# Optimization experiments

Hardware: AMD Instinct MI355X
Metric: run time of the kernel (lower is better)

Reference implementation:

```python
import jax, jax.numpy as jnp
import numpy as np

D_MODEL = 2048
N_HEADS = 16
D_HEAD = D_MODEL // N_HEADS
FF = 4 * D_MODEL
B, L = 2, 2048


def setup_inputs() -> dict:
    key = jax.random.key(0)
    ks = jax.random.split(key, 12)
    s = 0.02
    inp = {
        "x": jax.random.normal(ks[0], (B, L, D_MODEL), jnp.float32),
        "rope_cos": jnp.cos(jnp.arange(L)[:, None] / (10000.0 ** (jnp.arange(D_HEAD) / D_HEAD))).astype(jnp.float32),
        "rope_sin": jnp.sin(jnp.arange(L)[:, None] / (10000.0 ** (jnp.arange(D_HEAD) / D_HEAD))).astype(jnp.float32),
        "mask": jnp.ones((B, L), jnp.int32),
        "w_norm1": jnp.ones((D_MODEL,), jnp.float32),
        "w_norm2": jnp.ones((D_MODEL,), jnp.float32),
        # linear weights stored as [in, out] (transposed torch layout)
        "wq": jax.random.normal(ks[1], (D_MODEL, D_MODEL), jnp.float32) * s,
        "wk": jax.random.normal(ks[2], (D_MODEL, D_MODEL), jnp.float32) * s,
        "wv": jax.random.normal(ks[3], (D_MODEL, D_MODEL), jnp.float32) * s,
        "wo": jax.random.normal(ks[4], (D_MODEL, D_MODEL), jnp.float32) * s,
        "w_ff1": jax.random.normal(ks[5], (D_MODEL, FF), jnp.float32) * s,
        "w_ff2": jax.random.normal(ks[6], (FF, D_MODEL), jnp.float32) * s,
    }
    return inp


def _rmsnorm(x, w):
    eps = jnp.finfo(x.dtype).eps
    return x * jax.lax.rsqrt(jnp.mean(x * x, axis=-1, keepdims=True) + eps) * w


def _rotate_half(x):
    x1, x2 = jnp.split(x, 2, axis=-1)
    return jnp.concatenate([-x2, x1], axis=-1)


def reference(x, rope_cos, rope_sin, mask, w_norm1, w_norm2, wq, wk, wv, wo, w_ff1, w_ff2):
    b, l, d = x.shape
    h, dh = N_HEADS, D_HEAD

    residual = x
    xn = _rmsnorm(x, w_norm1)
    # project and split heads: [B, H, L, DH]
    q = (xn @ wq).reshape(b, l, h, dh).transpose(0, 2, 1, 3)
    k = (xn @ wk).reshape(b, l, h, dh).transpose(0, 2, 1, 3)
    v = (xn @ wv).reshape(b, l, h, dh).transpose(0, 2, 1, 3)

    cos = rope_cos[None, None]  # [1,1,L,DH]
    sin = rope_sin[None, None]
    q = q * cos + _rotate_half(q) * sin
    k = k * cos + _rotate_half(k) * sin

    scores = jnp.einsum("bhqd,bhkd->bhqk", q, k) * (dh ** -0.5)
    causal = jnp.tril(jnp.ones((l, l), bool))  # allowed positions
    allowed = causal[None, None] & (mask[:, None, None, :] != 0)
    scores = jnp.where(allowed, scores, -jnp.inf)
    attn = jax.nn.softmax(scores, axis=-1)  # dropout is identity in eval

    out = jnp.einsum("bhqk,bhkd->bhqd", attn, v)
    out = out.transpose(0, 2, 1, 3).reshape(b, l, d)
    x = residual + out @ wo

    xn2 = _rmsnorm(x, w_norm2)
    ff = jax.nn.silu(xn2 @ w_ff1) @ w_ff2
    return x + ff
```

## Files before the change

kernel.cpp:

```cpp
#include <hip/hip_runtime.h>


typedef __bf16 bf16;
typedef __bf16 bf16x8 __attribute__((ext_vector_type(8)));
typedef float  f32x4  __attribute__((ext_vector_type(4)));

__device__ __forceinline__ void gload16(const void* g, void* l) {
  __builtin_amdgcn_global_load_lds((const __attribute__((address_space(1))) void*)g,
                                   (__attribute__((address_space(3))) void*)l,
                                   16, 0, 0);
}

#define CBAR asm volatile("" ::: "memory")
#define WAITV(N) asm volatile("s_waitcnt vmcnt(" #N ")" ::: "memory")
#define LGKM0 asm volatile("s_waitcnt lgkmcnt(0)" ::: "memory")
#define BARR { CBAR; __builtin_amdgcn_s_barrier(); CBAR; }

__global__ __launch_bounds__(256) void rmsnorm_to_bf16(
    const float* __restrict__ x, const float* __restrict__ w, bf16* __restrict__ out)
{
  const int D = 2048;
  const int row = blockIdx.x;
  const int tid = threadIdx.x;
  const float* xr = x + (size_t)row * D;
  float4 a = ((const float4*)xr)[tid * 2];
  float4 c = ((const float4*)xr)[tid * 2 + 1];
  float ss = a.x*a.x + a.y*a.y + a.z*a.z + a.w*a.w
           + c.x*c.x + c.y*c.y + c.z*c.z + c.w*c.w;
  #pragma unroll
  for (int m = 1; m < 64; m <<= 1) ss += __shfl_xor(ss, m, 64);
  __shared__ float red[4];
  if ((tid & 63) == 0) red[tid >> 6] = ss;
  __syncthreads();
  float tot = red[0] + red[1] + red[2] + red[3];
  float rms = rsqrtf(tot * (1.0f / D) + 1.1920929e-7f);
  const float* wr = w + tid * 8;
  float vals[8] = {a.x, a.y, a.z, a.w, c.x, c.y, c.z, c.w};
  bf16x8 o;
  #pragma unroll
  for (int j = 0; j < 8; ++j) o[j] = (bf16)(vals[j] * rms * wr[j]);
  *(bf16x8*)(out + (size_t)row * D + tid * 8) = o;
}

__global__ __launch_bounds__(256) void transpose_to_bf16(
    const float* __restrict__ in, bf16* __restrict__ out, int R, int C)
{
  __shared__ float tile[32][33];
  const int tx = threadIdx.x, ty = threadIdx.y;
  const int c0 = blockIdx.x * 32, r0 = blockIdx.y * 32;
  #pragma unroll
  for (int i = 0; i < 4; ++i)
    tile[ty + i * 8][tx] = in[(size_t)(r0 + ty + i * 8) * C + c0 + tx];
  __syncthreads();
  #pragma unroll
  for (int i = 0; i < 4; ++i)
    out[(size_t)(c0 + ty + i * 8) * R + r0 + tx] = (bf16)tile[tx][ty + i * 8];
}

__global__ __launch_bounds__(256) void v_transpose(
    const bf16* __restrict__ v, bf16* __restrict__ vt)
{
  const int L = 2048, DM = 2048;
  __shared__ bf16 tile[32][33];
  const int tx = threadIdx.x, ty = threadIdx.y;
  const int k0 = blockIdx.x * 32;
  const int d0 = blockIdx.y * 32;
  const int bh = blockIdx.z;
  const int b = bh >> 4, h = bh & 15;
  #pragma unroll
  for (int i = 0; i < 4; ++i)
    tile[ty + i * 8][tx] = v[(size_t)(b * L + k0 + ty + i * 8) * DM + h * 128 + d0 + tx];
  __syncthreads();
  #pragma unroll
  for (int i = 0; i < 4; ++i) {
    const int d = d0 + ty + i * 8;
    const int key = k0 + tx;
    const int keysw = (key & ~63) | (((((key >> 3) & 7) ^ (d & 7)) << 3)) | (key & 7);
    vt[(size_t)(bh * 128 + d) * L + keysw] = tile[tx][ty + i * 8];
  }
}

template<int EPI>
__global__ __launch_bounds__(512, 2) void gemm256(
    const bf16* __restrict__ A, const bf16* __restrict__ Bt,
    void* Cout, const float* __restrict__ resid, int M, int N, int K)
{
  __shared__ bf16 sA[2][2][128 * 64];
  __shared__ bf16 sB[2][2][128 * 64];

  const int tid = threadIdx.x, lane = tid & 63, w = tid >> 6;
  const int wm = w >> 2, wn = w & 3;
  const int lo = lane & 15, hi = lane >> 4;
  const int lo7 = lo & 7;

  const int nbn = N >> 8;
  const int nwg = gridDim.x;
  int swz = blockIdx.x;
  if ((nwg & 7) == 0) { const int cpx = nwg >> 3; swz = (swz & 7) * cpx + (swz >> 3); }
  const int bm = swz / nbn, bn = swz % nbn;

  const int r0 = tid >> 3,         s0 = (tid & 7) ^ (r0 & 7);
  const int r1 = (512 + tid) >> 3, s1 = ((512 + tid) & 7) ^ (r1 & 7);
  const bf16* Ab = A  + (size_t)(bm * 256) * K;
  const bf16* Bb = Bt + (size_t)(bn * 256) * K;
  const size_t o0 = (size_t)r0 * K + s0 * 8;
  const size_t o1 = (size_t)r1 * K + s1 * 8;
  const int dst0 = (w * 64) * 8, dst1 = (512 + w * 64) * 8;
  const size_t rhK = (size_t)128 * K;

  bf16x8 afA[2][4], b0[2][2], b1[2][2];
  f32x4 acc[8][4] = {};
  const int NT = K >> 6;

  auto stageA = [&](int b, int rh, int kt) {
    const bf16* s = Ab + rh * rhK + (size_t)kt * 64;
    gload16(s + o0, &sA[b][rh][dst0]);
    gload16(s + o1, &sA[b][rh][dst1]);
  };
  auto stageB = [&](int b, int rh, int kt) {
    const bf16* s = Bb + rh * rhK + (size_t)kt * 64;
    gload16(s + o0, &sB[b][rh][dst0]);
    gload16(s + o1, &sB[b][rh][dst1]);
  };
  auto loadA = [&](int b, int rh) {
    #pragma unroll
    for (int ks = 0; ks < 2; ++ks)
      #pragma unroll
      for (int m = 0; m < 4; ++m) {
        const int row = wm * 64 + m * 16 + lo;
        afA[ks][m] = *(const bf16x8*)&sA[b][rh][row * 64 + (((ks * 4 + hi) ^ lo7) << 3)];
      }
  };
  auto loadB = [&](bf16x8 (&d)[2][2], int b, int rh) {
    #pragma unroll
    for (int ks = 0; ks < 2; ++ks)
      #pragma unroll
      for (int nj = 0; nj < 2; ++nj) {
        const int row = wn * 32 + nj * 16 + lo;
        d[ks][nj] = *(const bf16x8*)&sB[b][rh][row * 64 + (((ks * 4 + hi) ^ lo7) << 3)];
      }
  };
  auto mfma16 = [&](bf16x8 (&bf)[2][2], int mb, int nb2) {
    __builtin_amdgcn_s_setprio(1);
    #pragma unroll
    for (int ks = 0; ks < 2; ++ks)
      #pragma unroll
      for (int m = 0; m < 4; ++m)
        #pragma unroll
        for (int nj = 0; nj < 2; ++nj)
          acc[mb + m][nb2 + nj] = __builtin_amdgcn_mfma_f32_16x16x32_bf16(
              afA[ks][m], bf[ks][nj], acc[mb + m][nb2 + nj], 0, 0, 0);
    __builtin_amdgcn_s_setprio(0);
  };

  stageA(0, 0, 0); stageB(0, 0, 0); stageB(0, 1, 0); stageA(0, 1, 0);
  WAITV(4);
  BARR;

  for (int t = 0; t < NT; ++t) {
    const int buf = t & 1, nb = buf ^ 1;
    const bool st = (t + 1 < NT);
    loadA(buf, 0);
    loadB(b0, buf, 0);
    if (st) stageA(nb, 0, t + 1);
    BARR; LGKM0;
    mfma16(b0, 0, 0);
    if (st) { WAITV(4); } else { WAITV(0); }
    BARR;
    loadB(b1, buf, 1);
    if (st) stageB(nb, 0, t + 1);
    BARR; LGKM0;
    mfma16(b1, 0, 2);
    if (st) { WAITV(4); }
    BARR;
    loadA(buf, 1);
    if (st) stageB(nb, 1, t + 1);
    BARR; LGKM0;
    mfma16(b1, 4, 2);
    BARR;
    if (st) stageA(nb, 1, t + 1);
    BARR; LGKM0;
    mfma16(b0, 4, 0);
    if (st) { WAITV(4); }
    BARR;
  }

  #pragma unroll
  for (int mi = 0; mi < 8; ++mi) {
    #pragma unroll
    for (int j = 0; j < 4; ++j) {
      const size_t row = (size_t)(bm * 256 + (mi >> 2) * 128 + wm * 64 + (mi & 3) * 16 + hi * 4 + j);
      #pragma unroll
      for (int ni = 0; ni < 4; ++ni) {
        const int col = bn * 256 + (ni >> 1) * 128 + wn * 32 + (ni & 1) * 16 + lo;
        const float v = acc[mi][ni][j];
        if constexpr (EPI == 1) {
          ((float*)Cout)[row * (size_t)N + col] = v + resid[row * (size_t)N + col];
        } else if constexpr (EPI == 2) {
          ((bf16*)Cout)[row * (size_t)N + col] = (bf16)(v / (1.0f + __expf(-v)));
        } else {
          ((bf16*)Cout)[(size_t)(col >> 11) * 8388608 + row * 2048 + (col & 2047)] = (bf16)v;
        }
      }
    }
  }
}

template<int EPI>
__global__ __launch_bounds__(256, 2) void gemm_bt(
    const bf16* __restrict__ A, const bf16* __restrict__ Bt,
    void* Cout, const float* resid, int M, int N, int K)
{
  __shared__ bf16 sA[128 * 64];
  __shared__ bf16 sB[128 * 64];

  const int tid = threadIdx.x;
  const int lane = tid & 63;
  const int w = tid >> 6;
  const int wm = w >> 1, wn = w & 1;
  const int lo = lane & 15, hi = lane >> 4;

  const int nbn = N >> 7;
  const int nwg = gridDim.x;
  const int bid = blockIdx.x;
  int swz = bid;
  if ((nwg & 7) == 0) { const int cpx = nwg >> 3; swz = (bid & 7) * cpx + (bid >> 3); }
  const int bm = swz / nbn, bn = swz % nbn;

  const bf16* aptr[4];
  const bf16* bptr[4];
  #pragma unroll
  for (int i = 0; i < 4; ++i) {
    const int g = i * 256 + tid;
    const int row = g >> 3, gr = g & 7;
    aptr[i] = A  + (size_t)(bm * 128 + row) * K + gr * 8;
    bptr[i] = Bt + (size_t)(bn * 128 + row) * K + gr * 8;
  }

  f32x4 acc[4][4] = {};
  const int nkt = K >> 6;
  for (int kt = 0; kt < nkt; ++kt) {
    #pragma unroll
    for (int i = 0; i < 4; ++i) {
      gload16(aptr[i] + kt * 64, &sA[(i * 256 + w * 64) * 8]);
      gload16(bptr[i] + kt * 64, &sB[(i * 256 + w * 64) * 8]);
    }
    __syncthreads();
    #pragma unroll
    for (int ks = 0; ks < 2; ++ks) {
      bf16x8 af[4], bfm[4];
      #pragma unroll
      for (int mi = 0; mi < 4; ++mi)
        af[mi] = *(const bf16x8*)&sA[(wm * 64 + mi * 16 + lo) * 64 + ks * 32 + hi * 8];
      #pragma unroll
      for (int ni = 0; ni < 4; ++ni)
        bfm[ni] = *(const bf16x8*)&sB[(wn * 64 + ni * 16 + lo) * 64 + ks * 32 + hi * 8];
      #pragma unroll
      for (int mi = 0; mi < 4; ++mi)
        #pragma unroll
        for (int ni = 0; ni < 4; ++ni)
          acc[mi][ni] = __builtin_amdgcn_mfma_f32_16x16x32_bf16(af[mi], bfm[ni], acc[mi][ni], 0, 0, 0);
    }
    __syncthreads();
  }

  #pragma unroll
  for (int mi = 0; mi < 4; ++mi) {
    #pragma unroll
    for (int j = 0; j < 4; ++j) {
      const size_t row = (size_t)(bm * 128 + wm * 64 + mi * 16 + hi * 4 + j);
      const size_t ro = row * (size_t)N;
      #pragma unroll
      for (int ni = 0; ni < 4; ++ni) {
        const int col = bn * 128 + wn * 64 + ni * 16 + lo;
        const float v = acc[mi][ni][j];
        ((float*)Cout)[ro + col] = v + resid[ro + col];
      }
    }
  }
}

__global__ __launch_bounds__(256) void rope_qk(
    bf16* q, const bf16* __restrict__ k, bf16* __restrict__ kswz,
    const float* __restrict__ cs, const float* __restrict__ sn)
{
  const int L = 2048, DM = 2048;
  const int idx = blockIdx.x * 256 + threadIdx.x;
  const int m = idx >> 7;
  const int rem = idx & 127;
  const int h = rem >> 3, t8 = rem & 7;
  const int pos = m & (L - 1);
  const int d0 = t8 * 8;
  const float* cb = cs + (size_t)pos * 128 + d0;
  const float* sb = sn + (size_t)pos * 128 + d0;
  float4 c1a = *(const float4*)(cb);      float4 c1b = *(const float4*)(cb + 4);
  float4 c2a = *(const float4*)(cb + 64); float4 c2b = *(const float4*)(cb + 68);
  float4 s1a = *(const float4*)(sb);      float4 s1b = *(const float4*)(sb + 4);
  float4 s2a = *(const float4*)(sb + 64); float4 s2b = *(const float4*)(sb + 68);
  float c1[8] = {c1a.x,c1a.y,c1a.z,c1a.w,c1b.x,c1b.y,c1b.z,c1b.w};
  float c2[8] = {c2a.x,c2a.y,c2a.z,c2a.w,c2b.x,c2b.y,c2b.z,c2b.w};
  float s1[8] = {s1a.x,s1a.y,s1a.z,s1a.w,s1b.x,s1b.y,s1b.z,s1b.w};
  float s2[8] = {s2a.x,s2a.y,s2a.z,s2a.w,s2b.x,s2b.y,s2b.z,s2b.w};
  const size_t base = (size_t)m * DM + h * 128 + d0;

  {
    bf16x8 x1 = *(bf16x8*)(q + base);
    bf16x8 x2 = *(bf16x8*)(q + base + 64);
    bf16x8 o1, o2;
    #pragma unroll
    for (int j = 0; j < 8; ++j) {
      const float a = (float)x1[j], b = (float)x2[j];
      o1[j] = (bf16)(a * c1[j] - b * s1[j]);
      o2[j] = (bf16)(b * c2[j] + a * s2[j]);
    }
    *(bf16x8*)(q + base) = o1;
    *(bf16x8*)(q + base + 64) = o2;
  }
  {
    bf16x8 x1 = *(const bf16x8*)(k + base);
    bf16x8 x2 = *(const bf16x8*)(k + base + 64);
    bf16x8 o1, o2;
    #pragma unroll
    for (int j = 0; j < 8; ++j) {
      const float a = (float)x1[j], b = (float)x2[j];
      o1[j] = (bf16)(a * c1[j] - b * s1[j]);
      o2[j] = (bf16)(b * c2[j] + a * s2[j]);
    }
    const int s = pos & 15;
    const int p1 = t8 ^ s;
    const int p2 = (8 + t8) ^ s;
    bf16* kr = kswz + (size_t)m * DM + h * 128;
    *(bf16x8*)(kr + p1 * 8) = o1;
    *(bf16x8*)(kr + p2 * 8) = o2;
  }
}

__global__ __launch_bounds__(256, 2) void attn_fwd(
    const bf16* __restrict__ Q, const bf16* __restrict__ Kswz,
    const bf16* __restrict__ VT, const int* __restrict__ mask,
    bf16* __restrict__ O)
{
  const int L = 2048, DM = 2048;
  __shared__ bf16 Kt[2][64 * 128];
  __shared__ bf16 Vt[2][128 * 64];
  __shared__ bf16 Plds[4][16 * 64];

  const int tid = threadIdx.x, lane = tid & 63, w = tid >> 6;
  const int lo = lane & 15, hi = lane >> 4;
  const int s7 = lo & 7;
  const int n = blockIdx.x;
  const int xcd = n & 7, slot = n >> 3;
  const int bh = xcd + 8 * (slot >> 5);
  const int tile = 31 - (slot & 31);
  const int b = bh >> 4, h = bh & 15;
  const int qrow = tile * 64 + w * 16;
  const float scale = 0.08838834764831845f;
  const float NEG_INF = -__builtin_inff();

  bf16x8 qf[4];
  {
    const bf16* qb = Q + (size_t)(b * L + qrow + lo) * DM + h * 128;
    #pragma unroll
    for (int ds = 0; ds < 4; ++ds) qf[ds] = *(const bf16x8*)(qb + ds * 32 + hi * 8);
  }

  float mrow[4] = {NEG_INF, NEG_INF, NEG_INF, NEG_INF};
  float lrow[4] = {0.f, 0.f, 0.f, 0.f};
  f32x4 oacc[8] = {};

  const bf16* vsrc[4];
  const bf16* ksrc[4];
  #pragma unroll
  for (int i = 0; i < 4; ++i) {
    const int gv = i * 256 + tid;
    vsrc[i] = VT + (size_t)(bh * 128 + (gv >> 3)) * L + (gv & 7) * 8;
    const int gk = i * 256 + tid;
    ksrc[i] = Kswz + (size_t)(b * L + (gk >> 4)) * DM + h * 128 + (gk & 15) * 8;
  }

  #pragma unroll
  for (int i = 0; i < 4; ++i) {
    gload16(ksrc[i], &Kt[0][(i * 256 + w * 64) * 8]);
    gload16(vsrc[i], &Vt[0][(i * 256 + w * 64) * 8]);
  }
  __syncthreads();

  const int nkt = tile + 1;
  for (int kt = 0; kt < nkt; ++kt) {
    const int buf = kt & 1;
    if (kt + 1 < nkt) {
      #pragma unroll
      for (int i = 0; i < 4; ++i) {
        gload16(ksrc[i] + (size_t)(kt + 1) * 64 * DM, &Kt[buf ^ 1][(i * 256 + w * 64) * 8]);
        gload16(vsrc[i] + (kt + 1) * 64,              &Vt[buf ^ 1][(i * 256 + w * 64) * 8]);
      }
    }

    int mk[4];
    #pragma unroll
    for (int kb = 0; kb < 4; ++kb) mk[kb] = mask[b * L + kt * 64 + kb * 16 + lo];

    f32x4 S[4];
    __builtin_amdgcn_s_setprio(1);
    #pragma unroll
    for (int kb = 0; kb < 4; ++kb) {
      f32x4 s = {};
      #pragma unroll
      for (int ds = 0; ds < 4; ++ds) {
        const bf16x8 kf = *(const bf16x8*)&Kt[buf][(kb * 16 + lo) * 128 + (((ds * 4 + hi) ^ lo) * 8)];
        s = __builtin_amdgcn_mfma_f32_16x16x32_bf16(qf[ds], kf, s, 0, 0, 0);
      }
      S[kb] = s;
    }
    __builtin_amdgcn_s_setprio(0);

    #pragma unroll
    for (int kb = 0; kb < 4; ++kb) {
      const int kidx = kt * 64 + kb * 16 + lo;
      #pragma unroll
      for (int j = 0; j < 4; ++j) {
        const float sv = S[kb][j] * scale;
        S[kb][j] = (mk[kb] != 0 && kidx <= qrow + hi * 4 + j) ? sv : NEG_INF;
      }
    }

    float p[4][4];
    #pragma unroll
    for (int j = 0; j < 4; ++j) {
      float tm = fmaxf(fmaxf(S[0][j], S[1][j]), fmaxf(S[2][j], S[3][j]));
      tm = fmaxf(tm, __shfl_xor(tm, 1, 64));
      tm = fmaxf(tm, __shfl_xor(tm, 2, 64));
      tm = fmaxf(tm, __shfl_xor(tm, 4, 64));
      tm = fmaxf(tm, __shfl_xor(tm, 8, 64));
      const float mn = fmaxf(mrow[j], tm);
      const float mn2 = (mn == NEG_INF) ? 0.f : mn;
      const float alpha = __expf(mrow[j] - mn2);
      float ps = 0.f;
      #pragma unroll
      for (int kb = 0; kb < 4; ++kb) { p[kb][j] = __expf(S[kb][j] - mn2); ps += p[kb][j]; }
      ps += __shfl_xor(ps, 1, 64);
      ps += __shfl_xor(ps, 2, 64);
      ps += __shfl_xor(ps, 4, 64);
      ps += __shfl_xor(ps, 8, 64);
      lrow[j] = lrow[j] * alpha + ps;
      mrow[j] = mn;
      #pragma unroll
      for (int n2 = 0; n2 < 8; ++n2) oacc[n2][j] *= alpha;
    }

    #pragma unroll
    for (int kb = 0; kb < 4; ++kb)
      #pragma unroll
      for (int j = 0; j < 4; ++j) {
        const int row = hi * 4 + j;
        Plds[w][row * 64 + ((((kb * 2 + (lo >> 3)) ^ (row & 7))) << 3) + (lo & 7)] = (bf16)p[kb][j];
      }

    __builtin_amdgcn_s_setprio(1);
    #pragma unroll
    for (int ks = 0; ks < 2; ++ks) {
      const bf16x8 pa = *(const bf16x8*)&Plds[w][lo * 64 + (((ks * 4 + hi) ^ s7) << 3)];
      #pragma unroll
      for (int n2 = 0; n2 < 8; ++n2) {
        const int r = n2 * 16 + lo;
        const bf16x8 vf = *(const bf16x8*)&Vt[buf][r * 64 + (((ks * 4 + hi) ^ s7) << 3)];
        oacc[n2] = __builtin_amdgcn_mfma_f32_16x16x32_bf16(pa, vf, oacc[n2], 0, 0, 0);
      }
    }
    __builtin_amdgcn_s_setprio(0);

    __syncthreads();
  }

  float inv[4];
  #pragma unroll
  for (int j = 0; j < 4; ++j) inv[j] = (lrow[j] > 0.f) ? 1.f / lrow[j] : 0.f;
  bf16* ob = O + (size_t)(b * L + qrow) * DM + h * 128;
  #pragma unroll
  for (int n2 = 0; n2 < 8; ++n2)
    #pragma unroll
    for (int j = 0; j < 4; ++j)
      ob[(size_t)(hi * 4 + j) * DM + n2 * 16 + lo] = (bf16)(oacc[n2][j] * inv[j]);
}

extern "C" void kernel_launch(void* const* d_in, const int* in_sizes, int n_in,
                              void* d_out, int out_size, void* d_ws, size_t ws_size,
                              hipStream_t stream)
{
  (void)in_sizes; (void)n_in; (void)out_size; (void)ws_size;
  const float* x        = (const float*)d_in[0];
  const float* rope_cos = (const float*)d_in[1];
  const float* rope_sin = (const float*)d_in[2];
  const int*   mask     = (const int*)d_in[3];
  const float* w_norm1  = (const float*)d_in[4];
  const float* w_norm2  = (const float*)d_in[5];
  const float* wq       = (const float*)d_in[6];
  const float* wk       = (const float*)d_in[7];
  const float* wv       = (const float*)d_in[8];
  const float* wo       = (const float*)d_in[9];
  const float* w_ff1    = (const float*)d_in[10];
  const float* w_ff2    = (const float*)d_in[11];
  float* out = (float*)d_out;

  const int M = 4096, D = 2048, FFD = 8192;
  char* ws = (char*)d_ws;
  const size_t WSLAB = 8388608ull;
  const size_t XNB   = 16777216ull;
  bf16* wqt  = (bf16*)(ws);
  bf16* wkt  = (bf16*)(ws + WSLAB);
  bf16* wvt  = (bf16*)(ws + 2 * WSLAB);
  bf16* wot  = (bf16*)(ws + 3 * WSLAB);
  char* pool = ws + 4 * WSLAB;
  bf16* xn   = (bf16*)(pool);
  bf16* qb   = (bf16*)(pool + XNB);
  bf16* kb   = (bf16*)(pool + 2 * XNB);
  bf16* vb   = (bf16*)(pool + 3 * XNB);
  bf16* ao   = (bf16*)(pool + 4 * XNB);
  bf16* vt   = (bf16*)(pool);
  bf16* kswz = (bf16*)(pool + 3 * XNB);
  bf16* ff1t = (bf16*)(ws);
  bf16* hmid = (bf16*)(pool);
  bf16* ff2t = (bf16*)(ws);
  bf16* xn2  = (bf16*)(pool + 4 * XNB);

  const dim3 tb(32, 8);

  rmsnorm_to_bf16<<<M, 256, 0, stream>>>(x, w_norm1, xn);
  transpose_to_bf16<<<dim3(D / 32, D / 32), tb, 0, stream>>>(wq, wqt, D, D);
  transpose_to_bf16<<<dim3(D / 32, D / 32), tb, 0, stream>>>(wk, wkt, D, D);
  transpose_to_bf16<<<dim3(D / 32, D / 32), tb, 0, stream>>>(wv, wvt, D, D);
  transpose_to_bf16<<<dim3(D / 32, D / 32), tb, 0, stream>>>(wo, wot, D, D);

  gemm256<3><<<(M / 256) * (6144 / 256), 512, 0, stream>>>(xn, wqt, qb, nullptr, M, 6144, D);

  v_transpose<<<dim3(2048 / 32, 128 / 32, 32), tb, 0, stream>>>(vb, vt);

  rope_qk<<<2048, 256, 0, stream>>>(qb, kb, kswz, rope_cos, rope_sin);

  attn_fwd<<<1024, 256, 0, stream>>>(qb, kswz, vt, mask, ao);

  gemm_bt<1><<<(M / 128) * (D / 128), 256, 0, stream>>>(ao, wot, out, x, M, D, D);

  rmsnorm_to_bf16<<<M, 256, 0, stream>>>(out, w_norm2, xn2);

  transpose_to_bf16<<<dim3(FFD / 32, D / 32), tb, 0, stream>>>(w_ff1, ff1t, D, FFD);
  gemm256<2><<<(M / 256) * (FFD / 256), 512, 0, stream>>>(xn2, ff1t, hmid, nullptr, M, FFD, D);

  transpose_to_bf16<<<dim3(D / 32, FFD / 32), tb, 0, stream>>>(w_ff2, ff2t, FFD, D);
  gemm_bt<1><<<(M / 128) * (D / 128), 256, 0, stream>>>(hmid, ff2t, out, out, M, D, FFD);
}
```

Measured before the change: 749.2 us.

## Replace residual GEMMs with double-buffered swizzled 128x256 tile kernel

The two residual-add GEMMs (attention output projection and FF2) now use a new 512-thread kernel with 128x256 tiles instead of the old 256-thread 128x128 kernel. The new kernel double-buffers LDS, prefetches the next K tile while MFMAs run, XOR-swizzles LDS addressing to avoid bank conflicts, and raises wave priority around the MFMA blocks. The goal is to hide global-load latency and increase data reuse per tile. The tradeoff is half as many workgroups (256) on the N=2048 outputs, plus higher LDS use and register pressure.

```diff
diff --git a/kernel.cpp b/kernel.cpp
--- a/kernel.cpp
+++ b/kernel.cpp
@@ -194,9 +194,7 @@
       for (int ni = 0; ni < 4; ++ni) {
         const int col = bn * 256 + (ni >> 1) * 128 + wn * 32 + (ni & 1) * 16 + lo;
         const float v = acc[mi][ni][j];
-        if constexpr (EPI == 1) {
-          ((float*)Cout)[row * (size_t)N + col] = v + resid[row * (size_t)N + col];
-        } else if constexpr (EPI == 2) {
+        if constexpr (EPI == 2) {
           ((bf16*)Cout)[row * (size_t)N + col] = (bf16)(v / (1.0f + __expf(-v)));
         } else {
           ((bf16*)Cout)[(size_t)(col >> 11) * 8388608 + row * 2048 + (col & 2047)] = (bf16)v;
@@ -206,62 +204,98 @@
   }
 }
 
-template<int EPI>
-__global__ __launch_bounds__(256, 2) void gemm_bt(
+__global__ __launch_bounds__(512, 1) void gemm128(
     const bf16* __restrict__ A, const bf16* __restrict__ Bt,
-    void* Cout, const float* resid, int M, int N, int K)
-{
-  __shared__ bf16 sA[128 * 64];
-  __shared__ bf16 sB[128 * 64];
-
-  const int tid = threadIdx.x;
-  const int lane = tid & 63;
-  const int w = tid >> 6;
-  const int wm = w >> 1, wn = w & 1;
+    float* __restrict__ Cout, const float* __restrict__ resid, int M, int N, int K)
+{
+  __shared__ bf16 sA[2][128 * 64];
+  __shared__ bf16 sB[2][2][128 * 64];
+
+  const int tid = threadIdx.x, lane = tid & 63, w = tid >> 6;
+  const int wm = w >> 2, wn = w & 3;
   const int lo = lane & 15, hi = lane >> 4;
-
-  const int nbn = N >> 7;
+  const int lo7 = lo & 7;
+
+  const int nbn = N >> 8;
   const int nwg = gridDim.x;
-  const int bid = blockIdx.x;
-  int swz = bid;
-  if ((nwg & 7) == 0) { const int cpx = nwg >> 3; swz = (bid & 7) * cpx + (bid >> 3); }
+  int swz = blockIdx.x;
+  if ((nwg & 7) == 0) { const int cpx = nwg >> 3; swz = (swz & 7) * cpx + (swz >> 3); }
   const int bm = swz / nbn, bn = swz % nbn;
 
-  const bf16* aptr[4];
-  const bf16* bptr[4];
-  #pragma unroll
-  for (int i = 0; i < 4; ++i) {
-    const int g = i * 256 + tid;
-    const int row = g >> 3, gr = g & 7;
-    aptr[i] = A  + (size_t)(bm * 128 + row) * K + gr * 8;
-    bptr[i] = Bt + (size_t)(bn * 128 + row) * K + gr * 8;
-  }
-
+  const int r0 = tid >> 3,         s0 = (tid & 7) ^ (r0 & 7);
+  const int r1 = (512 + tid) >> 3, s1 = ((512 + tid) & 7) ^ (r1 & 7);
+  const bf16* Ab = A  + (size_t)(bm * 128) * K;
+  const bf16* Bb = Bt + (size_t)(bn * 256) * K;
+  const size_t o0 = (size_t)r0 * K + s0 * 8;
+  const size_t o1 = (size_t)r1 * K + s1 * 8;
+  const int dst0 = (w * 64) * 8, dst1 = (512 + w * 64) * 8;
+  const size_t nhK = (size_t)128 * K;
+
+  bf16x8 afA[2][4], b0[2][2], b1[2][2];
   f32x4 acc[4][4] = {};
-  const int nkt = K >> 6;
-  for (int kt = 0; kt < nkt; ++kt) {
-    #pragma unroll
-    for (int i = 0; i < 4; ++i) {
-      gload16(aptr[i] + kt * 64, &sA[(i * 256 + w * 64) * 8]);
-      gload16(bptr[i] + kt * 64, &sB[(i * 256 + w * 64) * 8]);
-    }
-    __syncthreads();
-    #pragma unroll
-    for (int ks = 0; ks < 2; ++ks) {
-      bf16x8 af[4], bfm[4];
-      #pragma unroll
-      for (int mi = 0; mi < 4; ++mi)
-        af[mi] = *(const bf16x8*)&sA[(wm * 64 + mi * 16 + lo) * 64 + ks * 32 + hi * 8];
-      #pragma unroll
-      for (int ni = 0; ni < 4; ++ni)
-        bfm[ni] = *(const bf16x8*)&sB[(wn * 64 + ni * 16 + lo) * 64 + ks * 32 + hi * 8];
-      #pragma unroll
-      for (int mi = 0; mi < 4; ++mi)
+  const int NT = K >> 6;
+
+  auto stageA = [&](int b, int kt) {
+    const bf16* s = Ab + (size_t)kt * 64;
+    gload16(s + o0, &sA[b][dst0]);
+    gload16(s + o1, &sA[b][dst1]);
+  };
+  auto stageB = [&](int b, int nh, int kt) {
+    const bf16* s = Bb + nh * nhK + (size_t)kt * 64;
+    gload16(s + o0, &sB[b][nh][dst0]);
+    gload16(s + o1, &sB[b][nh][dst1]);
+  };
+  auto loadA = [&](int b) {
+    #pragma unroll
+    for (int ks = 0; ks < 2; ++ks)
+      #pragma unroll
+      for (int m = 0; m < 4; ++m) {
+        const int row = wm * 64 + m * 16 + lo;
+        afA[ks][m] = *(const bf16x8*)&sA[b][row * 64 + (((ks * 4 + hi) ^ lo7) << 3)];
+      }
+  };
+  auto loadB = [&](bf16x8 (&d)[2][2], int b, int nh) {
+    #pragma unroll
+    for (int ks = 0; ks < 2; ++ks)
+      #pragma unroll
+      for (int nj = 0; nj < 2; ++nj) {
+        const int row = wn * 32 + nj * 16 + lo;
+        d[ks][nj] = *(const bf16x8*)&sB[b][nh][row * 64 + (((ks * 4 + hi) ^ lo7) << 3)];
+      }
+  };
+  auto mfma16 = [&](bf16x8 (&bf)[2][2], int nb2) {
+    __builtin_amdgcn_s_setprio(1);
+    #pragma unroll
+    for (int ks = 0; ks < 2; ++ks)
+      #pragma unroll
+      for (int m = 0; m < 4; ++m)
         #pragma unroll
-        for (int ni = 0; ni < 4; ++ni)
-          acc[mi][ni] = __builtin_amdgcn_mfma_f32_16x16x32_bf16(af[mi], bfm[ni], acc[mi][ni], 0, 0, 0);
-    }
-    __syncthreads();
+        for (int nj = 0; nj < 2; ++nj)
+          acc[m][nb2 + nj] = __builtin_amdgcn_mfma_f32_16x16x32_bf16(
+              afA[ks][m], bf[ks][nj], acc[m][nb2 + nj], 0, 0, 0);
+    __builtin_amdgcn_s_setprio(0);
+  };
+
+  stageA(0, 0); stageB(0, 0, 0); stageB(0, 1, 0);
+  WAITV(0);
+  BARR;
+
+  for (int t = 0; t < NT; ++t) {
+    const int buf = t & 1, nb = buf ^ 1;
+    const bool st = (t + 1 < NT);
+    loadA(buf);
+    loadB(b0, buf, 0);
+    if (st) stageA(nb, t + 1);
+    BARR; LGKM0;
+    mfma16(b0, 0);
+    if (st) { WAITV(2); } else { WAITV(0); }
+    BARR;
+    loadB(b1, buf, 1);
+    if (st) { stageB(nb, 0, t + 1); stageB(nb, 1, t + 1); }
+    BARR; LGKM0;
+    mfma16(b1, 2);
+    if (st) { WAITV(2); }
+    BARR;
   }
 
   #pragma unroll
@@ -272,9 +306,8 @@
       const size_t ro = row * (size_t)N;
       #pragma unroll
       for (int ni = 0; ni < 4; ++ni) {
-        const int col = bn * 128 + wn * 64 + ni * 16 + lo;
-        const float v = acc[mi][ni][j];
-        ((float*)Cout)[ro + col] = v + resid[ro + col];
+        const int col = bn * 256 + (ni >> 1) * 128 + wn * 32 + (ni & 1) * 16 + lo;
+        Cout[ro + col] = acc[mi][ni][j] + resid[ro + col];
       }
     }
   }
@@ -539,7 +572,7 @@
 
   attn_fwd<<<1024, 256, 0, stream>>>(qb, kswz, vt, mask, ao);
 
-  gemm_bt<1><<<(M / 128) * (D / 128), 256, 0, stream>>>(ao, wot, out, x, M, D, D);
+  gemm128<<<(M / 128) * (D / 256), 512, 0, stream>>>(ao, wot, out, x, M, D, D);
 
   rmsnorm_to_bf16<<<M, 256, 0, stream>>>(out, w_norm2, xn2);
 
@@ -547,5 +580,5 @@
   gemm256<2><<<(M / 256) * (FFD / 256), 512, 0, stream>>>(xn2, ff1t, hmid, nullptr, M, FFD, D);
 
   transpose_to_bf16<<<dim3(D / 32, FFD / 32), tb, 0, stream>>>(w_ff2, ff2t, FFD, D);
-  gemm_bt<1><<<(M / 128) * (D / 128), 256, 0, stream>>>(hmid, ff2t, out, out, M, D, FFD);
-}
+  gemm128<<<(M / 128) * (D / 256), 512, 0, stream>>>(hmid, ff2t, out, out, M, D, FFD);
+}
```

New measurement: 674.3 us. -10.0%, faster.
